# Kernel tuning notes

Measured on AMD Instinct MI355X. Metric: run time of the kernel, lower is better.

## Reference

```python
import jax, jax.numpy as jnp
import numpy as np
import math

B, N, W = 8, 2048, 512

def setup_inputs() -> dict:
    key0 = jax.random.key(0)
    ks = jax.random.split(key0, 6)
    return {
        "query": jax.random.normal(ks[0], (B, N, W), dtype=jnp.float32),
        "key":   jax.random.normal(ks[1], (B, N, W), dtype=jnp.float32),
        "W1": jax.random.normal(ks[2], (W, W), dtype=jnp.float32) * (1.0 / math.sqrt(W)),
        "b1": jax.random.normal(ks[3], (W,), dtype=jnp.float32) * 0.01,
        "W2": jax.random.normal(ks[4], (W, W), dtype=jnp.float32) * (1.0 / math.sqrt(W)),
        "b2": jax.random.normal(ks[5], (W,), dtype=jnp.float32) * 0.01,
    }

def _attn(q, k, v):
    # scores: [B, N, N]
    d_k = q.shape[-1]
    scores = jnp.einsum('bnd,bmd->bnm', q, k) / jnp.sqrt(jnp.asarray(d_k, q.dtype))
    p = jax.nn.softmax(scores, axis=-1)
    return jnp.einsum('bnm,bmd->bnd', p, v)

def reference(query, key, W1, b1, W2, b2):
    # nn.Linear: x @ W.T + b
    q = jnp.einsum('bnd,ed->bne', query, W1) + b1
    k = jnp.einsum('bnd,ed->bne', key, W2) + b2
    x1 = _attn(q, k, q)  # attention(query, key, query)
    x2 = _attn(k, q, k)  # attention(key, query, key)
    return jnp.concatenate((x1, x2), axis=1)  # [B, 2N, W]
```

## Files before the change

kernel.cpp:

```cpp
#include <hip/hip_runtime.h>
#include <hip/hip_bf16.h>
#include <stdint.h>

typedef unsigned short ushort_t;
typedef __attribute__((ext_vector_type(8))) short short8;
typedef __attribute__((ext_vector_type(4))) short short4v;
typedef __attribute__((ext_vector_type(4))) float f32x4;

__device__ inline ushort_t f2bf(float x) {
  uint32_t u = __float_as_uint(x);
  u += 0x7fffu + ((u >> 16) & 1u);
  return (ushort_t)(u >> 16);
}
__device__ inline float bfu2f(uint32_t h) { return __uint_as_float(h << 16); }

__device__ inline uint32_t pk2bf(float a, float b) {
  __hip_bfloat162 h = __float22bfloat162_rn(make_float2(a, b));
  union { __hip_bfloat162 h2; uint32_t u; } cv; cv.h2 = h; return cv.u;
}

__device__ inline void gload_lds16(const void* g, void* l) {
  __builtin_amdgcn_global_load_lds((const __attribute__((address_space(1))) uint32_t*)g,
                                   (__attribute__((address_space(3))) uint32_t*)l, 16, 0, 0);
}

__global__ __launch_bounds__(256) void linear_kernel(
    const float* __restrict__ query, const float* __restrict__ key,
    const float* __restrict__ W1, const float* __restrict__ b1,
    const float* __restrict__ W2, const float* __restrict__ b2,
    ushort_t* __restrict__ q_bf, ushort_t* __restrict__ k_bf,
    ushort_t* __restrict__ qT, ushort_t* __restrict__ kT)
{
  __shared__ __attribute__((aligned(16))) char smraw[34816];
  float*    smF = (float*)smraw;
  ushort_t* smU = (ushort_t*)smraw;

  int bx = blockIdx.x;
  int which = bx >> 9, r2 = bx & 511, ct = r2 & 3, rt = r2 >> 2;
  const float* X    = which ? key : query;
  const float* Wm   = which ? W2  : W1;
  const float* bias = which ? b2  : b1;
  ushort_t* OUT  = which ? k_bf : q_bf;
  ushort_t* OUTT = which ? kT   : qT;

  int t = threadIdx.x, w = t >> 6, lane = t & 63, g = lane >> 4, m = lane & 15;
  int wr = (w >> 1) * 64, wc = (w & 1) * 64;
  int sr = lane >> 3, sp = lane & 7, sc = sp ^ sr;

  f32x4 zero = {0.f, 0.f, 0.f, 0.f};
  f32x4 acc[4][4];
#pragma unroll
  for (int i = 0; i < 4; ++i)
#pragma unroll
    for (int j = 0; j < 4; ++j) acc[i][j] = zero;

  for (int d0 = 0; d0 < 512; d0 += 32) {
    __syncthreads();
#pragma unroll
    for (int i = 0; i < 8; ++i) {
      int qi = w * 8 + i;
      const float* gsrc;
      float* ldst;
      if (qi < 16) {
        gsrc = X + (size_t)(rt * 128 + qi * 8 + sr) * 512 + d0 + sc * 4;
        ldst = smF + qi * 256;
      } else {
        int s = qi - 16;
        gsrc = Wm + (size_t)(ct * 128 + s * 8 + sr) * 512 + d0 + sc * 4;
        ldst = smF + 4096 + s * 256;
      }
      gload_lds16(gsrc, ldst);
    }
    __syncthreads();

    short8 a4[4], b4[4];
#pragma unroll
    for (int i = 0; i < 4; ++i) {
      int row = wr + 16 * i + m, r8 = row & 7;
      int base = (row >> 3) * 256 + r8 * 32;
      f32x4 lo = *(const f32x4*)&smF[base + (((2 * g)     ^ r8) * 4)];
      f32x4 hi = *(const f32x4*)&smF[base + (((2 * g + 1) ^ r8) * 4)];
      union { uint32_t u[4]; short8 s; } fr;
      fr.u[0] = pk2bf(lo[0], lo[1]); fr.u[1] = pk2bf(lo[2], lo[3]);
      fr.u[2] = pk2bf(hi[0], hi[1]); fr.u[3] = pk2bf(hi[2], hi[3]);
      a4[i] = fr.s;
    }
#pragma unroll
    for (int j = 0; j < 4; ++j) {
      int row = wc + 16 * j + m, r8 = row & 7;
      int base = 4096 + (row >> 3) * 256 + r8 * 32;
      f32x4 lo = *(const f32x4*)&smF[base + (((2 * g)     ^ r8) * 4)];
      f32x4 hi = *(const f32x4*)&smF[base + (((2 * g + 1) ^ r8) * 4)];
      union { uint32_t u[4]; short8 s; } fr;
      fr.u[0] = pk2bf(lo[0], lo[1]); fr.u[1] = pk2bf(lo[2], lo[3]);
      fr.u[2] = pk2bf(hi[0], hi[1]); fr.u[3] = pk2bf(hi[2], hi[3]);
      b4[j] = fr.s;
    }
#pragma unroll
    for (int i = 0; i < 4; ++i)
#pragma unroll
      for (int j = 0; j < 4; ++j)
        acc[i][j] = __builtin_amdgcn_mfma_f32_16x16x32_bf16(a4[i], b4[j], acc[i][j], 0, 0, 0);
  }
  __syncthreads();

  float bw[4];
#pragma unroll
  for (int j = 0; j < 4; ++j) bw[j] = bias[ct * 128 + wc + 16 * j + m];

#pragma unroll
  for (int j = 0; j < 4; ++j)
#pragma unroll
    for (int i = 0; i < 4; ++i) {
      f32x4 c4 = acc[i][j];
#pragma unroll
      for (int rr = 0; rr < 4; ++rr)
        smU[(wr + 16 * i + 4 * g + rr) * 136 + wc + 16 * j + m] = f2bf(c4[rr] + bw[j]);
    }
  __syncthreads();
  {
    int row = t >> 1, half = t & 1;
    size_t gb = (size_t)(rt * 128 + row) * 512 + ct * 128 + half * 64;
#pragma unroll
    for (int i = 0; i < 8; ++i)
      *(short8*)(OUT + gb + i * 8) = *(const short8*)&smU[row * 136 + half * 64 + i * 8];
  }
  __syncthreads();

#pragma unroll
  for (int j = 0; j < 4; ++j)
#pragma unroll
    for (int i = 0; i < 4; ++i) {
      f32x4 c4 = acc[i][j];
      short4v tv;
#pragma unroll
      for (int rr = 0; rr < 4; ++rr) tv[rr] = (short)f2bf(c4[rr] + bw[j]);
      *(short4v*)&smU[(wc + 16 * j + m) * 136 + wr + 16 * i + 4 * g] = tv;
    }
  __syncthreads();
  {
    int cC = t >> 1, half = t & 1;
    size_t b_ = (size_t)(rt >> 4);
    size_t gb = b_ * (512 * 2048) + (size_t)(ct * 128 + cC) * 2048
              + (size_t)(rt & 15) * 128 + half * 64;
#pragma unroll
    for (int i = 0; i < 8; ++i)
      *(short8*)(OUTT + gb + i * 8) = *(const short8*)&smU[cC * 136 + half * 64 + i * 8];
  }
}

__global__ __launch_bounds__(512) void attn_kernel(
    const ushort_t* __restrict__ qb, const ushort_t* __restrict__ kb_,
    const ushort_t* __restrict__ qT, const ushort_t* __restrict__ kT,
    float* __restrict__ out)
{
  extern __shared__ ushort_t sm[];
  const float CEXP = 1.4426950408889634f / 22.62741699796952f;

  int bx = blockIdx.x;
  int group = bx & 15, mtile = bx >> 4;
  int b = group >> 1, att = group & 1;
  const ushort_t* Qp = (att ? kb_ : qb) + (size_t)b * (2048 * 512);
  const ushort_t* Kp = (att ? qb  : kb_) + (size_t)b * (2048 * 512);
  const ushort_t* Vt = (att ? kT  : qT)  + (size_t)b * (512 * 2048);

  int t = threadIdx.x, w = t >> 6, lane = t & 63, g = lane >> 4, m = lane & 15;
  int qrow = mtile * 128 + w * 16 + m;
  int sw8  = ((g ^ ((m >> 1) & 3)) * 8);
  int srow = lane >> 2;
  int soff = ((lane & 3) ^ ((lane >> 3) & 3)) * 8;

  short8 qf[16];
#pragma unroll
  for (int ks = 0; ks < 16; ++ks)
    qf[ks] = *(const short8*)(Qp + (size_t)qrow * 512 + ks * 32 + g * 8);

  f32x4 zero = {0.f, 0.f, 0.f, 0.f};
  f32x4 acc[32];
#pragma unroll
  for (int dt = 0; dt < 32; ++dt) acc[dt] = zero;
  float l = 0.f;

  auto stage = [&](int buf, int kb) {
    ushort_t* base = sm + buf * 32768;
    const int kbase = kb * 32;
#pragma unroll
    for (int i = 0; i < 4; ++i) {
      int qi = w * 4 + i, ks = qi >> 1, tt2 = qi & 1;
      const ushort_t* gsrc = Kp + (size_t)(kbase + tt2 * 16 + srow) * 512 + ks * 32 + soff;
      gload_lds16(gsrc, base + ks * 1024 + tt2 * 512);
    }
#pragma unroll
    for (int i = 0; i < 4; ++i) {
      int qi = w * 4 + i;
      const ushort_t* gsrc = Vt + (size_t)(qi * 16 + srow) * 2048 + kbase + soff;
      gload_lds16(gsrc, base + 16384 + qi * 512);
    }
  };

  stage(0, 0);

  for (int kb = 0; kb < 64; ++kb) {
    int cur = kb & 1;
    __syncthreads();
    if (kb + 1 < 64) stage(1 - cur, kb + 1);
    const ushort_t* base = sm + cur * 32768;

    f32x4 T0 = zero, T1 = zero;
#pragma unroll
    for (int ks = 0; ks < 16; ++ks) {
      short8 k0 = *(const short8*)&base[ks * 1024 +       m * 32 + sw8];
      short8 k1 = *(const short8*)&base[ks * 1024 + 512 + m * 32 + sw8];
      T0 = __builtin_amdgcn_mfma_f32_16x16x32_bf16(k0, qf[ks], T0, 0, 0, 0);
      T1 = __builtin_amdgcn_mfma_f32_16x16x32_bf16(k1, qf[ks], T1, 0, 0, 0);
    }

    uint32_t h[8];
#pragma unroll
    for (int r = 0; r < 4; ++r) {
      float e0 = __builtin_amdgcn_exp2f(T0[r] * CEXP);
      float e1 = __builtin_amdgcn_exp2f(T1[r] * CEXP);
      h[r]     = f2bf(e0);
      h[4 + r] = f2bf(e1);
      l += bfu2f(h[r]) + bfu2f(h[4 + r]);
    }
    int dw0 = (int)(h[0] | (h[1] << 16));
    int dw1 = (int)(h[2] | (h[3] << 16));
    int dw2 = (int)(h[4] | (h[5] << 16));
    int dw3 = (int)(h[6] | (h[7] << 16));

    int sA = ((2 * g) & 3) * 16 + m, sB = sA + 16;
    int A0 = __shfl(dw0, sA, 64), A1 = __shfl(dw1, sA, 64);
    int A2 = __shfl(dw2, sA, 64), A3 = __shfl(dw3, sA, 64);
    int B0 = __shfl(dw0, sB, 64), B1 = __shfl(dw1, sB, 64);
    int B2 = __shfl(dw2, sB, 64), B3 = __shfl(dw3, sB, 64);
    bool hi = (g >= 2);
    union { int i4[4]; short8 s; } pu;
    pu.i4[0] = hi ? A2 : A0; pu.i4[1] = hi ? A3 : A1;
    pu.i4[2] = hi ? B2 : B0; pu.i4[3] = hi ? B3 : B1;
    short8 pfrag = pu.s;

#pragma unroll
    for (int dt = 0; dt < 32; ++dt) {
      short8 vf = *(const short8*)&base[16384 + dt * 512 + m * 32 + sw8];
      acc[dt] = __builtin_amdgcn_mfma_f32_16x16x32_bf16(vf, pfrag, acc[dt], 0, 0, 0);
    }
  }

  l += __shfl_xor(l, 16, 64);
  l += __shfl_xor(l, 32, 64);
  float inv = 1.0f / l;
  size_t orow = (size_t)b * 4096 + (size_t)att * 2048 + mtile * 128 + w * 16 + m;
  float* obase = out + orow * 512;
#pragma unroll
  for (int dt = 0; dt < 32; ++dt) {
    f32x4 v = acc[dt] * inv;
    *(f32x4*)(obase + dt * 16 + g * 4) = v;
  }
}

extern "C" void kernel_launch(void* const* d_in, const int* in_sizes, int n_in,
                              void* d_out, int out_size, void* d_ws, size_t ws_size,
                              hipStream_t stream) {
  const float* query = (const float*)d_in[0];
  const float* key   = (const float*)d_in[1];
  const float* W1    = (const float*)d_in[2];
  const float* b1    = (const float*)d_in[3];
  const float* W2    = (const float*)d_in[4];
  const float* b2    = (const float*)d_in[5];
  float* out = (float*)d_out;

  ushort_t* ws   = (ushort_t*)d_ws;
  ushort_t* q_bf = ws;
  ushort_t* k_bf = ws + 8388608;
  ushort_t* qT   = ws + 16777216;
  ushort_t* kT   = ws + 25165824;

  (void)hipFuncSetAttribute((const void*)attn_kernel,
                            hipFuncAttributeMaxDynamicSharedMemorySize, 131072);

  linear_kernel<<<1024, 256, 0, stream>>>(query, key, W1, b1, W2, b2,
                                          q_bf, k_bf, qT, kT);
  attn_kernel<<<256, 512, 131072, stream>>>(q_bf, k_bf, qT, kT, out);
}
```

Measured before the change: 333.8 us.

## Double-buffer linear GEMM, remap blocks, and share P tiles across wave pairs in attention

The linear kernel now double-buffers its fp32 tiles in dynamic shared memory so the next k-slice loads while the current one computes. It also remaps block indices, apparently to improve cache locality. In the attention kernel, each wave writes its bf16 probability tile to LDS and then computes a 32-row by 256-column output slab with pairs of waves, replacing the shuffle-based fragment build. This halves the V fragments each wave reads per key block. The change also adds s_setprio hints around the MFMA loops and launch_bounds(512,2), at the cost of an extra block-wide barrier per iteration and a larger LDS footprint.

```diff
diff --git a/kernel.cpp b/kernel.cpp
--- a/kernel.cpp
+++ b/kernel.cpp
@@ -31,11 +31,13 @@
     ushort_t* __restrict__ q_bf, ushort_t* __restrict__ k_bf,
     ushort_t* __restrict__ qT, ushort_t* __restrict__ kT)
 {
-  __shared__ __attribute__((aligned(16))) char smraw[34816];
+  extern __shared__ __attribute__((aligned(16))) char smraw[];
   float*    smF = (float*)smraw;
   ushort_t* smU = (ushort_t*)smraw;
 
-  int bx = blockIdx.x;
+  int bx0 = blockIdx.x;
+  int bx = ((bx0 & 7) << 7) | (bx0 >> 3);
+
   int which = bx >> 9, r2 = bx & 511, ct = r2 & 3, rt = r2 >> 2;
   const float* X    = which ? key : query;
   const float* Wm   = which ? W2  : W1;
@@ -54,8 +56,8 @@
 #pragma unroll
     for (int j = 0; j < 4; ++j) acc[i][j] = zero;
 
-  for (int d0 = 0; d0 < 512; d0 += 32) {
-    __syncthreads();
+  auto stage = [&](int buf, int d0) {
+    float* dst = smF + buf * 8192;
 #pragma unroll
     for (int i = 0; i < 8; ++i) {
       int qi = w * 8 + i;
@@ -63,23 +65,31 @@
       float* ldst;
       if (qi < 16) {
         gsrc = X + (size_t)(rt * 128 + qi * 8 + sr) * 512 + d0 + sc * 4;
-        ldst = smF + qi * 256;
+        ldst = dst + qi * 256;
       } else {
         int s = qi - 16;
         gsrc = Wm + (size_t)(ct * 128 + s * 8 + sr) * 512 + d0 + sc * 4;
-        ldst = smF + 4096 + s * 256;
+        ldst = dst + 4096 + s * 256;
       }
       gload_lds16(gsrc, ldst);
     }
+  };
+
+  stage(0, 0);
+
+  for (int it = 0; it < 16; ++it) {
+    int cur = it & 1;
     __syncthreads();
+    if (it + 1 < 16) stage(1 - cur, (it + 1) * 32);
+    const float* bufF = smF + cur * 8192;
 
     short8 a4[4], b4[4];
 #pragma unroll
     for (int i = 0; i < 4; ++i) {
       int row = wr + 16 * i + m, r8 = row & 7;
       int base = (row >> 3) * 256 + r8 * 32;
-      f32x4 lo = *(const f32x4*)&smF[base + (((2 * g)     ^ r8) * 4)];
-      f32x4 hi = *(const f32x4*)&smF[base + (((2 * g + 1) ^ r8) * 4)];
+      f32x4 lo = *(const f32x4*)&bufF[base + (((2 * g)     ^ r8) * 4)];
+      f32x4 hi = *(const f32x4*)&bufF[base + (((2 * g + 1) ^ r8) * 4)];
       union { uint32_t u[4]; short8 s; } fr;
       fr.u[0] = pk2bf(lo[0], lo[1]); fr.u[1] = pk2bf(lo[2], lo[3]);
       fr.u[2] = pk2bf(hi[0], hi[1]); fr.u[3] = pk2bf(hi[2], hi[3]);
@@ -89,8 +99,8 @@
     for (int j = 0; j < 4; ++j) {
       int row = wc + 16 * j + m, r8 = row & 7;
       int base = 4096 + (row >> 3) * 256 + r8 * 32;
-      f32x4 lo = *(const f32x4*)&smF[base + (((2 * g)     ^ r8) * 4)];
-      f32x4 hi = *(const f32x4*)&smF[base + (((2 * g + 1) ^ r8) * 4)];
+      f32x4 lo = *(const f32x4*)&bufF[base + (((2 * g)     ^ r8) * 4)];
+      f32x4 hi = *(const f32x4*)&bufF[base + (((2 * g + 1) ^ r8) * 4)];
       union { uint32_t u[4]; short8 s; } fr;
       fr.u[0] = pk2bf(lo[0], lo[1]); fr.u[1] = pk2bf(lo[2], lo[3]);
       fr.u[2] = pk2bf(hi[0], hi[1]); fr.u[3] = pk2bf(hi[2], hi[3]);
@@ -149,7 +159,7 @@
   }
 }
 
-__global__ __launch_bounds__(512) void attn_kernel(
+__global__ __launch_bounds__(512, 2) void attn_kernel(
     const ushort_t* __restrict__ qb, const ushort_t* __restrict__ kb_,
     const ushort_t* __restrict__ qT, const ushort_t* __restrict__ kT,
     float* __restrict__ out)
@@ -165,10 +175,20 @@
   const ushort_t* Vt = (att ? kT  : qT)  + (size_t)b * (512 * 2048);
 
   int t = threadIdx.x, w = t >> 6, lane = t & 63, g = lane >> 4, m = lane & 15;
+  int wq = w >> 1, dh = w & 1;
   int qrow = mtile * 128 + w * 16 + m;
   int sw8  = ((g ^ ((m >> 1) & 3)) * 8);
   int srow = lane >> 2;
   int soff = ((lane & 3) ^ ((lane >> 3) & 3)) * 8;
+  int pm6 = (m & 6);
+
+  ushort_t* Plds = sm + 65536;
+  float* lbuf = (float*)(sm + 69632);
+
+  int pw0 = (w * 16 + m) * 32 + ((g ^ pm6) << 2);
+  int pw1 = (w * 16 + m) * 32 + (((g + 4) ^ pm6) << 2);
+  int pr0 = (wq * 32 +      m) * 32 + (((2 * g) ^ pm6) << 2);
+  int pr1 = (wq * 32 + 16 + m) * 32 + (((2 * g) ^ pm6) << 2);
 
   short8 qf[16];
 #pragma unroll
@@ -176,9 +196,9 @@
     qf[ks] = *(const short8*)(Qp + (size_t)qrow * 512 + ks * 32 + g * 8);
 
   f32x4 zero = {0.f, 0.f, 0.f, 0.f};
-  f32x4 acc[32];
-#pragma unroll
-  for (int dt = 0; dt < 32; ++dt) acc[dt] = zero;
+  f32x4 acc[16][2];
+#pragma unroll
+  for (int dt = 0; dt < 16; ++dt) { acc[dt][0] = zero; acc[dt][1] = zero; }
   float l = 0.f;
 
   auto stage = [&](int buf, int kb) {
@@ -207,6 +227,7 @@
     const ushort_t* base = sm + cur * 32768;
 
     f32x4 T0 = zero, T1 = zero;
+    __builtin_amdgcn_s_setprio(1);
 #pragma unroll
     for (int ks = 0; ks < 16; ++ks) {
       short8 k0 = *(const short8*)&base[ks * 1024 +       m * 32 + sw8];
@@ -214,6 +235,7 @@
       T0 = __builtin_amdgcn_mfma_f32_16x16x32_bf16(k0, qf[ks], T0, 0, 0, 0);
       T1 = __builtin_amdgcn_mfma_f32_16x16x32_bf16(k1, qf[ks], T1, 0, 0, 0);
     }
+    __builtin_amdgcn_s_setprio(0);
 
     uint32_t h[8];
 #pragma unroll
@@ -224,38 +246,45 @@
       h[4 + r] = f2bf(e1);
       l += bfu2f(h[r]) + bfu2f(h[4 + r]);
     }
-    int dw0 = (int)(h[0] | (h[1] << 16));
-    int dw1 = (int)(h[2] | (h[3] << 16));
-    int dw2 = (int)(h[4] | (h[5] << 16));
-    int dw3 = (int)(h[6] | (h[7] << 16));
-
-    int sA = ((2 * g) & 3) * 16 + m, sB = sA + 16;
-    int A0 = __shfl(dw0, sA, 64), A1 = __shfl(dw1, sA, 64);
-    int A2 = __shfl(dw2, sA, 64), A3 = __shfl(dw3, sA, 64);
-    int B0 = __shfl(dw0, sB, 64), B1 = __shfl(dw1, sB, 64);
-    int B2 = __shfl(dw2, sB, 64), B3 = __shfl(dw3, sB, 64);
-    bool hi = (g >= 2);
-    union { int i4[4]; short8 s; } pu;
-    pu.i4[0] = hi ? A2 : A0; pu.i4[1] = hi ? A3 : A1;
-    pu.i4[2] = hi ? B2 : B0; pu.i4[3] = hi ? B3 : B1;
-    short8 pfrag = pu.s;
-
-#pragma unroll
-    for (int dt = 0; dt < 32; ++dt) {
-      short8 vf = *(const short8*)&base[16384 + dt * 512 + m * 32 + sw8];
-      acc[dt] = __builtin_amdgcn_mfma_f32_16x16x32_bf16(vf, pfrag, acc[dt], 0, 0, 0);
-    }
+    uint2 p0, p1;
+    p0.x = h[0] | (h[1] << 16); p0.y = h[2] | (h[3] << 16);
+    p1.x = h[4] | (h[5] << 16); p1.y = h[6] | (h[7] << 16);
+    *(uint2*)&Plds[pw0] = p0;
+    *(uint2*)&Plds[pw1] = p1;
+
+    __syncthreads();
+
+    short8 pf0 = *(const short8*)&Plds[pr0];
+    short8 pf1 = *(const short8*)&Plds[pr1];
+    __builtin_amdgcn_s_setprio(1);
+#pragma unroll
+    for (int dt = 0; dt < 16; ++dt) {
+      short8 vf = *(const short8*)&base[16384 + (dh * 16 + dt) * 512 + m * 32 + sw8];
+      acc[dt][0] = __builtin_amdgcn_mfma_f32_16x16x32_bf16(vf, pf0, acc[dt][0], 0, 0, 0);
+      acc[dt][1] = __builtin_amdgcn_mfma_f32_16x16x32_bf16(vf, pf1, acc[dt][1], 0, 0, 0);
+    }
+    __builtin_amdgcn_s_setprio(0);
   }
 
   l += __shfl_xor(l, 16, 64);
   l += __shfl_xor(l, 32, 64);
-  float inv = 1.0f / l;
-  size_t orow = (size_t)b * 4096 + (size_t)att * 2048 + mtile * 128 + w * 16 + m;
-  float* obase = out + orow * 512;
-#pragma unroll
-  for (int dt = 0; dt < 32; ++dt) {
-    f32x4 v = acc[dt] * inv;
-    *(f32x4*)(obase + dt * 16 + g * 4) = v;
+  if (lane < 16) lbuf[w * 16 + lane] = 1.0f / l;
+  __syncthreads();
+
+  float inv0 = lbuf[wq * 32 + m];
+  float inv1 = lbuf[wq * 32 + 16 + m];
+  size_t orow0 = (size_t)b * 4096 + (size_t)att * 2048 + mtile * 128 + wq * 32 + m;
+  float* ob0 = out + orow0 * 512 + dh * 256;
+  float* ob1 = out + (orow0 + 16) * 512 + dh * 256;
+#pragma unroll
+  for (int dt = 0; dt < 16; ++dt) {
+    f32x4 v0 = acc[dt][0] * inv0;
+    *(f32x4*)(ob0 + dt * 16 + g * 4) = v0;
+  }
+#pragma unroll
+  for (int dt = 0; dt < 16; ++dt) {
+    f32x4 v1 = acc[dt][1] * inv1;
+    *(f32x4*)(ob1 + dt * 16 + g * 4) = v1;
   }
 }
 
@@ -276,10 +305,12 @@
   ushort_t* qT   = ws + 16777216;
   ushort_t* kT   = ws + 25165824;
 
+  (void)hipFuncSetAttribute((const void*)linear_kernel,
+                            hipFuncAttributeMaxDynamicSharedMemorySize, 65536);
   (void)hipFuncSetAttribute((const void*)attn_kernel,
-                            hipFuncAttributeMaxDynamicSharedMemorySize, 131072);
-
-  linear_kernel<<<1024, 256, 0, stream>>>(query, key, W1, b1, W2, b2,
-                                          q_bf, k_bf, qT, kT);
-  attn_kernel<<<256, 512, 131072, stream>>>(q_bf, k_bf, qT, kT, out);
-}
+                            hipFuncAttributeMaxDynamicSharedMemorySize, 139776);
+
+  linear_kernel<<<1024, 256, 65536, stream>>>(query, key, W1, b1, W2, b2,
+                                              q_bf, k_bf, qT, kT);
+  attn_kernel<<<256, 512, 139776, stream>>>(q_bf, k_bf, qT, kT, out);
+}
```

Result: faster. 311.0 us (-6.8%).
